# Performance work log

Hardware: AMD Instinct MI355X
Metric: run time of the kernel (lower is better)

The kernel has to match this reference:

```python
import jax, jax.numpy as jnp
import numpy as np

N_NODES = 50000
N_EDGES = 800000
F_IN = 128
HID = 32
HEADS = 4
N_CLASSES = 16
N_GRAPHS = 64
EPS = 1e-5
NEG_SLOPE = 0.2


def setup_inputs() -> dict:
    key = jax.random.key(0)
    ks = jax.random.split(key, 12)
    x = jax.random.normal(ks[0], (N_NODES, F_IN), dtype=jnp.float32)
    edge_index = jax.random.randint(ks[1], (2, N_EDGES), 0, N_NODES, dtype=jnp.int64)
    batch = jnp.sort(jax.random.randint(ks[2], (N_NODES,), 0, N_GRAPHS, dtype=jnp.int64))
    # GATConv 1: F_IN -> HID per head, HEADS heads, concat
    W1 = jax.random.normal(ks[3], (F_IN, HEADS * HID), dtype=jnp.float32) / np.sqrt(F_IN)
    att_src1 = jax.random.normal(ks[4], (HEADS, HID), dtype=jnp.float32) / np.sqrt(HID)
    att_dst1 = jax.random.normal(ks[5], (HEADS, HID), dtype=jnp.float32) / np.sqrt(HID)
    bias1 = jnp.zeros((HEADS * HID,), dtype=jnp.float32)
    # GATConv 2: HEADS*HID -> N_CLASSES, 1 head, no concat
    W2 = jax.random.normal(ks[6], (HEADS * HID, N_CLASSES), dtype=jnp.float32) / np.sqrt(HEADS * HID)
    att_src2 = jax.random.normal(ks[7], (1, N_CLASSES), dtype=jnp.float32) / np.sqrt(N_CLASSES)
    att_dst2 = jax.random.normal(ks[8], (1, N_CLASSES), dtype=jnp.float32) / np.sqrt(N_CLASSES)
    bias2 = jnp.zeros((N_CLASSES,), dtype=jnp.float32)
    # BatchNorm affine params
    bn1_gamma = jnp.ones((F_IN,), dtype=jnp.float32)
    bn1_beta = jnp.zeros((F_IN,), dtype=jnp.float32)
    bn2_gamma = jnp.ones((HEADS * HID,), dtype=jnp.float32)
    bn2_beta = jnp.zeros((HEADS * HID,), dtype=jnp.float32)
    return dict(x=x, W1=W1, att_src1=att_src1, att_dst1=att_dst1, bias1=bias1,
                W2=W2, att_src2=att_src2, att_dst2=att_dst2, bias2=bias2,
                bn1_gamma=bn1_gamma, bn1_beta=bn1_beta,
                bn2_gamma=bn2_gamma, bn2_beta=bn2_beta,
                edge_index=edge_index, batch=batch)


def batchnorm(x, gamma, beta):
    mean = x.mean(axis=0)
    var = ((x - mean) ** 2).mean(axis=0)  # biased var, as torch BN uses for normalization
    return (x - mean) * jax.lax.rsqrt(var + EPS) * gamma + beta


def gat_conv(x, ei, W, a_src, a_dst, bias, heads, out_c, concat):
    N = x.shape[0]
    # add self loops (PyG default)
    loops = jnp.arange(N, dtype=ei.dtype)
    src = jnp.concatenate([ei[0], loops])
    dst = jnp.concatenate([ei[1], loops])
    h = (x @ W).reshape(N, heads, out_c)               # [N,H,C]
    a_s = (h * a_src).sum(-1)                          # [N,H]
    a_d = (h * a_dst).sum(-1)                          # [N,H]
    e = jax.nn.leaky_relu(a_s[src] + a_d[dst], NEG_SLOPE)  # [E,H]
    # softmax over incoming edges of each destination node
    emax = jax.ops.segment_max(e, dst, num_segments=N)[dst]
    ex = jnp.exp(e - emax)
    denom = jax.ops.segment_sum(ex, dst, num_segments=N)[dst]
    alpha = ex / denom                                  # [E,H]
    msg = h[src] * alpha[:, :, None]                    # [E,H,C]
    out = jax.ops.segment_sum(msg, dst, num_segments=N)  # [N,H,C]
    out = out.reshape(N, heads * out_c) if concat else out.mean(axis=1)
    return out + bias


def reference(x, W1, att_src1, att_dst1, bias1, W2, att_src2, att_dst2, bias2,
              bn1_gamma, bn1_beta, bn2_gamma, bn2_beta, edge_index, batch):
    h = batchnorm(x, bn1_gamma, bn1_beta)
    h = gat_conv(h, edge_index, W1, att_src1, att_dst1, bias1, HEADS, HID, True)
    h = jax.nn.relu(h)
    h = batchnorm(h, bn2_gamma, bn2_beta)
    h = gat_conv(h, edge_index, W2, att_src2, att_dst2, bias2, 1, N_CLASSES, False)
    h = jax.nn.gelu(h)
    # global mean pool over graphs
    sums = jax.ops.segment_sum(h, batch, num_segments=N_GRAPHS)
    counts = jax.ops.segment_sum(jnp.ones((h.shape[0],), h.dtype), batch, num_segments=N_GRAPHS)
    pooled = sums / jnp.maximum(counts, 1.0)[:, None]
    return jax.nn.log_softmax(pooled, axis=1)
```

## Files before the change

kernel.cpp:

```cpp
#include <hip/hip_runtime.h>
#include <math.h>
#include <stdint.h>

#define NN 50000
#define NE 800000
#define NG 64
#define NEG_SLOPE 0.2f
#define NBLK ((NN + 255) / 256)

typedef unsigned short u16;
typedef __attribute__((ext_vector_type(8))) unsigned short ushort8;
typedef __attribute__((ext_vector_type(8))) short short8v;
typedef __attribute__((ext_vector_type(4))) float f32x4;

__device__ __forceinline__ float lrelu(float x) { return x > 0.f ? x : NEG_SLOPE * x; }
__device__ __forceinline__ float bf2f(u16 u) { return __uint_as_float(((unsigned)u) << 16); }
__device__ __forceinline__ u16 f2bf(float f) {
    unsigned b = __float_as_uint(f);
    return (u16)((b + 0x7FFF + ((b >> 16) & 1)) >> 16);
}

__global__ __launch_bounds__(256) void col_stats_kernel(const float* __restrict__ X, int nrows,
                                                        float* __restrict__ sum, float* __restrict__ ssum) {
    int tid = threadIdx.x;
    int c = tid & 127, half = tid >> 7;
    int rows_per = (nrows + gridDim.x - 1) / gridDim.x;
    int r0 = blockIdx.x * rows_per;
    int r1 = r0 + rows_per; if (r1 > nrows) r1 = nrows;
    float s = 0.f, ss = 0.f;
    for (int r = r0 + half; r < r1; r += 2) {
        float v = X[(size_t)r * 128 + c];
        s += v; ss += v * v;
    }
    __shared__ float sm1[256], sm2[256];
    sm1[tid] = s; sm2[tid] = ss;
    __syncthreads();
    if (tid < 128) {
        s = sm1[tid] + sm1[tid + 128];
        ss = sm2[tid] + sm2[tid + 128];
        atomicAdd(&sum[c], s);
        atomicAdd(&ssum[c], ss);
    }
}

__global__ __launch_bounds__(128) void bn_prep1_kernel(const float* __restrict__ sum, const float* __restrict__ ssum,
                                                       const float* __restrict__ gamma, const float* __restrict__ beta,
                                                       const float* __restrict__ W, float inv_n,
                                                       u16* __restrict__ WpT, float* __restrict__ hb) {
    int k = threadIdx.x;
    float mean = sum[k] * inv_n;
    float var = ssum[k] * inv_n - mean * mean;
    float a = gamma[k] * rsqrtf(var + 1e-5f);
    float b = beta[k] - mean * a;
    for (int j = 0; j < 128; j++) WpT[j * 128 + k] = f2bf(a * W[k * 128 + j]);
    __shared__ float bs[128];
    bs[k] = b;
    __syncthreads();
    float acc = 0.f;
    for (int kk = 0; kk < 128; kk++) acc += bs[kk] * W[kk * 128 + k];
    hb[k] = acc;
}

__global__ __launch_bounds__(128) void bn_prep_kernel(const float* __restrict__ sum, const float* __restrict__ ssum,
                                                      const float* __restrict__ gamma, const float* __restrict__ beta,
                                                      const float* __restrict__ W, int J, float inv_n,
                                                      float* __restrict__ Wp, float* __restrict__ hb) {
    int k = threadIdx.x;
    float mean = sum[k] * inv_n;
    float var = ssum[k] * inv_n - mean * mean;
    float a = gamma[k] * rsqrtf(var + 1e-5f);
    float b = beta[k] - mean * a;
    for (int j = 0; j < J; j++) Wp[k * J + j] = a * W[k * J + j];
    __shared__ float bs[128];
    bs[k] = b;
    __syncthreads();
    if (k < J) {
        float acc = 0.f;
        for (int kk = 0; kk < 128; kk++) acc += bs[kk] * W[kk * J + k];
        hb[k] = acc;
    }
}

__global__ __launch_bounds__(256) void gemm1_mfma_kernel(const float* __restrict__ X, const u16* __restrict__ WpT,
                                                         const float* __restrict__ hbias, const float* __restrict__ atts,
                                                         const float* __restrict__ attd, u16* __restrict__ Hb,
                                                         float* __restrict__ as_o, float* __restrict__ ad_o) {
    __shared__ u16 wlds[128][136];
    int tid = threadIdx.x;
    for (int u = tid; u < 2048; u += 256) {
        int c = u >> 4, ch = u & 15;
        *(ushort8*)&wlds[c][ch * 8] = *(const ushort8*)&WpT[c * 128 + ch * 8];
    }
    int lane = tid & 63;
    int wv = tid >> 6;
    int cl = lane & 15;
    int kg = lane >> 4;
    int row_base = blockIdx.x * 64 + wv * 16;
    int rr = min(row_base + cl, NN - 1);

    short8v afrag[4];
#pragma unroll
    for (int kb = 0; kb < 4; kb++) {
        const float* xp = &X[(size_t)rr * 128 + kb * 32 + kg * 8];
        float4 x0 = *(const float4*)xp;
        float4 x1 = *(const float4*)(xp + 4);
        ushort8 t;
        t[0] = f2bf(x0.x); t[1] = f2bf(x0.y); t[2] = f2bf(x0.z); t[3] = f2bf(x0.w);
        t[4] = f2bf(x1.x); t[5] = f2bf(x1.y); t[6] = f2bf(x1.z); t[7] = f2bf(x1.w);
        afrag[kb] = (short8v)t;
    }
    __syncthreads();

    f32x4 acc[8];
#pragma unroll
    for (int ct = 0; ct < 8; ct++) {
        f32x4 a = {0.f, 0.f, 0.f, 0.f};
#pragma unroll
        for (int kb = 0; kb < 4; kb++) {
            ushort8 bv = *(const ushort8*)&wlds[ct * 16 + cl][kb * 32 + kg * 8];
            a = __builtin_amdgcn_mfma_f32_16x16x32_bf16(afrag[kb], (short8v)bv, a, 0, 0, 0);
        }
        acc[ct] = a;
    }

#pragma unroll
    for (int reg = 0; reg < 4; reg++) {
        int r = row_base + kg * 4 + reg;
        bool valid = (r < NN);
        float sp[4] = {0.f, 0.f, 0.f, 0.f}, dp[4] = {0.f, 0.f, 0.f, 0.f};
#pragma unroll
        for (int ct = 0; ct < 8; ct++) {
            int c = ct * 16 + cl;
            float v = acc[ct][reg] + hbias[c];
            if (valid) Hb[(size_t)r * 128 + c] = f2bf(v);
            sp[ct >> 1] += v * atts[c];
            dp[ct >> 1] += v * attd[c];
        }
#pragma unroll
        for (int off = 1; off < 16; off <<= 1) {
#pragma unroll
            for (int h = 0; h < 4; h++) {
                sp[h] += __shfl_xor(sp[h], off);
                dp[h] += __shfl_xor(dp[h], off);
            }
        }
        if (valid) {
            if (cl < 4) as_o[r * 4 + cl] = sp[cl];
            else if (cl < 8) ad_o[r * 4 + (cl - 4)] = dp[cl - 4];
        }
    }
}

__global__ __launch_bounds__(256) void deg_hist_kernel(const int* __restrict__ dst, int* __restrict__ deg, int ne) {
    int e = blockIdx.x * 256 + threadIdx.x;
    if (e < ne) atomicAdd(&deg[dst[e]], 1);
}

__global__ __launch_bounds__(256) void scan_part_kernel(const int* __restrict__ deg, int* __restrict__ blocksum) {
    int i = blockIdx.x * 256 + threadIdx.x;
    int d = (i < NN) ? deg[i] : 0;
#pragma unroll
    for (int off = 1; off < 64; off <<= 1) d += __shfl_xor(d, off);
    __shared__ int sm[4];
    if ((threadIdx.x & 63) == 0) sm[threadIdx.x >> 6] = d;
    __syncthreads();
    if (threadIdx.x == 0) blocksum[blockIdx.x] = sm[0] + sm[1] + sm[2] + sm[3];
}

__global__ __launch_bounds__(256) void scan_block_kernel(const int* __restrict__ blocksum, int* __restrict__ blockoff) {
    __shared__ int sm[256];
    int tid = threadIdx.x;
    int v = (tid < NBLK) ? blocksum[tid] : 0;
    sm[tid] = v;
    __syncthreads();
    for (int off = 1; off < 256; off <<= 1) {
        int t = (tid >= off) ? sm[tid - off] : 0;
        __syncthreads();
        sm[tid] += t;
        __syncthreads();
    }
    if (tid < NBLK) blockoff[tid] = sm[tid] - v;
}

__global__ __launch_bounds__(256) void scan_final_kernel(const int* __restrict__ deg, const int* __restrict__ blockoff,
                                                         int* __restrict__ rowptr, int* __restrict__ cursor) {
    __shared__ int sm[256];
    int tid = threadIdx.x;
    int i = blockIdx.x * 256 + tid;
    int d = (i < NN) ? deg[i] : 0;
    sm[tid] = d;
    __syncthreads();
    for (int off = 1; off < 256; off <<= 1) {
        int t = (tid >= off) ? sm[tid - off] : 0;
        __syncthreads();
        sm[tid] += t;
        __syncthreads();
    }
    int excl = sm[tid] - d + blockoff[blockIdx.x];
    if (i < NN) { rowptr[i] = excl; cursor[i] = excl; }
    if (i == NN - 1) rowptr[NN] = excl + d;
}

__global__ __launch_bounds__(256) void scatter_kernel(const int* __restrict__ src, const int* __restrict__ dst,
                                                      int* __restrict__ cursor, int* __restrict__ csr_src, int ne) {
    int e = blockIdx.x * 256 + threadIdx.x;
    if (e < ne) {
        int d = dst[e];
        int pos = atomicAdd(&cursor[d], 1);
        csr_src[pos] = src[e];
    }
}

__global__ __launch_bounds__(256) void gat1_agg_kernel(const u16* __restrict__ Hb, const float* __restrict__ as1,
                                                       const float* __restrict__ ad1, const int* __restrict__ rowptr,
                                                       const int* __restrict__ csr_src, const float* __restrict__ bias1,
                                                       float* __restrict__ out) {
    int n = blockIdx.x * 4 + (threadIdx.x >> 6);
    int lane = threadIdx.x & 63;
    int quarter = lane >> 4;
    int within = lane & 15;
    int head = within >> 2;
    int c8 = within * 8;
    int start = rowptr[n], end = rowptr[n + 1];

    float4 ad4 = *(const float4*)&ad1[n * 4];
    float4 as4 = *(const float4*)&as1[n * 4];
    float ps0 = __expf(lrelu(as4.x + ad4.x));
    float ps1 = __expf(lrelu(as4.y + ad4.y));
    float ps2 = __expf(lrelu(as4.z + ad4.z));
    float ps3 = __expf(lrelu(as4.w + ad4.w));
    float pselfh = (head == 0) ? ps0 : (head == 1) ? ps1 : (head == 2) ? ps2 : ps3;

    float acc[8];
    {
        ushort8 hv = *(const ushort8*)&Hb[(size_t)n * 128 + c8];
        float w = (quarter == 0) ? pselfh : 0.f;
#pragma unroll
        for (int k = 0; k < 8; k++) acc[k] = w * bf2f(hv[k]);
    }
    float d0 = 0.f, d1 = 0.f, d2 = 0.f, d3 = 0.f;

    for (int base = start; base < end; base += 64) {
        int i = base + lane;
        int s = 0;
        float p0 = 0.f, p1 = 0.f, p2 = 0.f, p3 = 0.f;
        if (i < end) {
            s = csr_src[i];
            float4 a = *(const float4*)&as1[(size_t)s * 4];
            p0 = __expf(lrelu(a.x + ad4.x));
            p1 = __expf(lrelu(a.y + ad4.y));
            p2 = __expf(lrelu(a.z + ad4.z));
            p3 = __expf(lrelu(a.w + ad4.w));
            d0 += p0; d1 += p1; d2 += p2; d3 += p3;
        }
        int cnt = min(64, end - base);
#pragma unroll 2
        for (int j = 0; j < cnt; j += 4) {
            int jj = j + quarter;
            int s0 = __shfl(s, jj);
            float q0 = __shfl(p0, jj);
            float q1 = __shfl(p1, jj);
            float q2 = __shfl(p2, jj);
            float q3 = __shfl(p3, jj);
            float pp = (head == 0) ? q0 : (head == 1) ? q1 : (head == 2) ? q2 : q3;
            if (jj < cnt) {
                ushort8 hv = *(const ushort8*)&Hb[(size_t)s0 * 128 + c8];
#pragma unroll
                for (int k = 0; k < 8; k++) acc[k] += pp * bf2f(hv[k]);
            }
        }
    }

#pragma unroll
    for (int off = 1; off < 64; off <<= 1) {
        d0 += __shfl_xor(d0, off);
        d1 += __shfl_xor(d1, off);
        d2 += __shfl_xor(d2, off);
        d3 += __shfl_xor(d3, off);
    }
    float den = ((head == 0) ? d0 : (head == 1) ? d1 : (head == 2) ? d2 : d3) + pselfh;
#pragma unroll
    for (int k = 0; k < 8; k++) {
        acc[k] += __shfl_xor(acc[k], 16);
        acc[k] += __shfl_xor(acc[k], 32);
    }
    if (quarter == 0) {
        float inv = 1.f / den;
        float4 b0 = *(const float4*)&bias1[c8];
        float4 b1 = *(const float4*)&bias1[c8 + 4];
        float4 o0, o1;
        o0.x = fmaxf(acc[0] * inv + b0.x, 0.f);
        o0.y = fmaxf(acc[1] * inv + b0.y, 0.f);
        o0.z = fmaxf(acc[2] * inv + b0.z, 0.f);
        o0.w = fmaxf(acc[3] * inv + b0.w, 0.f);
        o1.x = fmaxf(acc[4] * inv + b1.x, 0.f);
        o1.y = fmaxf(acc[5] * inv + b1.y, 0.f);
        o1.z = fmaxf(acc[6] * inv + b1.z, 0.f);
        o1.w = fmaxf(acc[7] * inv + b1.w, 0.f);
        *(float4*)&out[(size_t)n * 128 + c8] = o0;
        *(float4*)&out[(size_t)n * 128 + c8 + 4] = o1;
    }
}

__global__ __launch_bounds__(256) void gemm2_kernel(const float* __restrict__ X, const float* __restrict__ Wp,
                                                    const float* __restrict__ hb, const float* __restrict__ atts,
                                                    const float* __restrict__ attd, float* __restrict__ H2,
                                                    float* __restrict__ as_o, float* __restrict__ ad_o) {
    __shared__ float xs[16][129];
    __shared__ float wsm[128][16];
    __shared__ float hbs[16], ats[16], atd[16];
    int tid = threadIdx.x;
    if (tid < 16) { hbs[tid] = hb[tid]; ats[tid] = atts[tid]; atd[tid] = attd[tid]; }
    for (int u = tid; u < 2048; u += 256) wsm[u >> 4][u & 15] = Wp[u];
    int r0 = blockIdx.x * 16;
    for (int u = tid; u < 2048; u += 256) {
        int row = u >> 7, cc = u & 127;
        xs[row][cc] = X[(size_t)(r0 + row) * 128 + cc];
    }
    __syncthreads();
    int r = tid >> 4, c = tid & 15;
    float acc = 0.f;
#pragma unroll 8
    for (int k = 0; k < 128; k++) acc += xs[r][k] * wsm[k][c];
    acc += hbs[c];
    H2[(size_t)(r0 + r) * 16 + c] = acc;
    float s = acc * ats[c], d = acc * atd[c];
#pragma unroll
    for (int off = 1; off < 16; off <<= 1) {
        s += __shfl_xor(s, off);
        d += __shfl_xor(d, off);
    }
    if (c == 0) { as_o[r0 + r] = s; ad_o[r0 + r] = d; }
}

__global__ __launch_bounds__(256) void gat2_agg_kernel(const float* __restrict__ H2, const float* __restrict__ as2,
                                                       const float* __restrict__ ad2, const int* __restrict__ rowptr,
                                                       const int* __restrict__ csr_src, const float* __restrict__ bias2,
                                                       float* __restrict__ out) {
    int n = blockIdx.x * 4 + (threadIdx.x >> 6);
    int lane = threadIdx.x & 63;
    int quarter = lane >> 4;
    int c = lane & 15;
    int start = rowptr[n], end = rowptr[n + 1];
    float adn = ad2[n], asn = as2[n];
    float pself = __expf(lrelu(asn + adn));

    float acc = (quarter == 0) ? pself * H2[(size_t)n * 16 + c] : 0.f;
    float d = 0.f;

    for (int base = start; base < end; base += 64) {
        int i = base + lane;
        int s = 0;
        float p = 0.f;
        if (i < end) {
            s = csr_src[i];
            p = __expf(lrelu(as2[s] + adn));
            d += p;
        }
        int cnt = min(64, end - base);
#pragma unroll 2
        for (int j = 0; j < cnt; j += 4) {
            int jj = j + quarter;
            int s0 = __shfl(s, jj);
            float q = __shfl(p, jj);
            if (jj < cnt) acc += q * H2[(size_t)s0 * 16 + c];
        }
    }
#pragma unroll
    for (int off = 1; off < 64; off <<= 1) d += __shfl_xor(d, off);
    float den = d + pself;
    acc += __shfl_xor(acc, 16);
    acc += __shfl_xor(acc, 32);

    if (quarter == 0) {
        float xo = acc / den + bias2[c];
        float t = tanhf(0.7978845608028654f * (xo + 0.044715f * xo * xo * xo));
        out[(size_t)n * 16 + c] = 0.5f * xo * (1.f + t);
    }
}

__global__ __launch_bounds__(256) void pool_lsm_kernel(const float* __restrict__ X, const int* __restrict__ batch,
                                                       int nn, float* __restrict__ out) {
    int g = blockIdx.x;
    int tid = threadIdx.x;
    int lo = 0, hi = nn;
    while (lo < hi) { int mid = (lo + hi) >> 1; if (batch[mid] < g) lo = mid + 1; else hi = mid; }
    int s = lo;
    lo = s; hi = nn;
    while (lo < hi) { int mid = (lo + hi) >> 1; if (batch[mid] < g + 1) lo = mid + 1; else hi = mid; }
    int e2 = lo;
    int c = tid & 15, grp = tid >> 4;
    float acc = 0.f;
    for (int r = s + grp; r < e2; r += 16) acc += X[(size_t)r * 16 + c];
    __shared__ float sm[256];
    sm[tid] = acc;
    __syncthreads();
    for (int off = 8; off >= 1; off >>= 1) {
        if (grp < off) sm[tid] += sm[tid + off * 16];
        __syncthreads();
    }
    if (tid < 16) {
        float cnt = (float)(e2 - s);
        float v = sm[tid] / fmaxf(cnt, 1.f);
        float mx = v;
        mx = fmaxf(mx, __shfl_xor(mx, 1));
        mx = fmaxf(mx, __shfl_xor(mx, 2));
        mx = fmaxf(mx, __shfl_xor(mx, 4));
        mx = fmaxf(mx, __shfl_xor(mx, 8));
        float ex = __expf(v - mx);
        float ssum = ex;
        ssum += __shfl_xor(ssum, 1);
        ssum += __shfl_xor(ssum, 2);
        ssum += __shfl_xor(ssum, 4);
        ssum += __shfl_xor(ssum, 8);
        out[g * 16 + tid] = v - mx - __logf(ssum);
    }
}

extern "C" void kernel_launch(void* const* d_in, const int* in_sizes, int n_in,
                              void* d_out, int out_size, void* d_ws, size_t ws_size,
                              hipStream_t stream) {
    const float* x        = (const float*)d_in[0];
    const float* W1       = (const float*)d_in[1];
    const float* att_src1 = (const float*)d_in[2];
    const float* att_dst1 = (const float*)d_in[3];
    const float* bias1    = (const float*)d_in[4];
    const float* W2       = (const float*)d_in[5];
    const float* att_src2 = (const float*)d_in[6];
    const float* att_dst2 = (const float*)d_in[7];
    const float* bias2    = (const float*)d_in[8];
    const float* bn1g     = (const float*)d_in[9];
    const float* bn1b     = (const float*)d_in[10];
    const float* bn2g     = (const float*)d_in[11];
    const float* bn2b     = (const float*)d_in[12];
    const int*   ei       = (const int*)d_in[13];
    const int*   batch    = (const int*)d_in[14];
    float* out = (float*)d_out;

    char* p = (char*)d_ws;
    auto alloc = [&](size_t bytes) -> char* {
        char* r = p;
        p += (bytes + 255) & ~(size_t)255;
        return r;
    };
    float* bnbuf   = (float*)alloc(512 * sizeof(float));
    int*   deg     = (int*)alloc(NN * sizeof(int));
    int*   rowptr  = (int*)alloc((NN + 1) * sizeof(int));
    int*   cursor  = (int*)alloc(NN * sizeof(int));
    int*   csr_src = (int*)alloc(NE * sizeof(int));
    int*   blocksum= (int*)alloc(NBLK * sizeof(int));
    int*   blockoff= (int*)alloc(NBLK * sizeof(int));
    u16*   W1pT    = (u16*)alloc(128 * 128 * sizeof(u16));
    float* h1bias  = (float*)alloc(128 * sizeof(float));
    u16*   h1b     = (u16*)alloc((size_t)NN * 128 * sizeof(u16));
    float* as1     = (float*)alloc((size_t)NN * 4 * sizeof(float));
    float* ad1     = (float*)alloc((size_t)NN * 4 * sizeof(float));
    float* out1    = (float*)alloc((size_t)NN * 128 * sizeof(float));
    float* W2p     = (float*)alloc(128 * 16 * sizeof(float));
    float* h2bias  = (float*)alloc(16 * sizeof(float));
    float* h2      = (float*)alloc((size_t)NN * 16 * sizeof(float));
    float* as2     = (float*)alloc(NN * sizeof(float));
    float* ad2     = (float*)alloc(NN * sizeof(float));
    float* out2g   = (float*)alloc((size_t)NN * 16 * sizeof(float));

    float* bn1sum = bnbuf;
    float* bn1ss  = bnbuf + 128;
    float* bn2sum = bnbuf + 256;
    float* bn2ss  = bnbuf + 384;
    const int* esrc = ei;
    const int* edst = ei + NE;

    hipMemsetAsync(bnbuf, 0, 512 * sizeof(float) + NN * sizeof(int), stream);

    const float inv_n = 1.f / (float)NN;

    col_stats_kernel<<<256, 256, 0, stream>>>(x, NN, bn1sum, bn1ss);
    bn_prep1_kernel<<<1, 128, 0, stream>>>(bn1sum, bn1ss, bn1g, bn1b, W1, inv_n, W1pT, h1bias);
    gemm1_mfma_kernel<<<(NN + 63) / 64, 256, 0, stream>>>(x, W1pT, h1bias, att_src1, att_dst1, h1b, as1, ad1);
    deg_hist_kernel<<<(NE + 255) / 256, 256, 0, stream>>>(edst, deg, NE);
    scan_part_kernel<<<NBLK, 256, 0, stream>>>(deg, blocksum);
    scan_block_kernel<<<1, 256, 0, stream>>>(blocksum, blockoff);
    scan_final_kernel<<<NBLK, 256, 0, stream>>>(deg, blockoff, rowptr, cursor);
    scatter_kernel<<<(NE + 255) / 256, 256, 0, stream>>>(esrc, edst, cursor, csr_src, NE);
    gat1_agg_kernel<<<NN / 4, 256, 0, stream>>>(h1b, as1, ad1, rowptr, csr_src, bias1, out1);
    col_stats_kernel<<<256, 256, 0, stream>>>(out1, NN, bn2sum, bn2ss);
    bn_prep_kernel<<<1, 128, 0, stream>>>(bn2sum, bn2ss, bn2g, bn2b, W2, 16, inv_n, W2p, h2bias);
    gemm2_kernel<<<NN / 16, 256, 0, stream>>>(out1, W2p, h2bias, att_src2, att_dst2, h2, as2, ad2);
    gat2_agg_kernel<<<NN / 4, 256, 0, stream>>>(h2, as2, ad2, rowptr, csr_src, bias2, out2g);
    pool_lsm_kernel<<<NG, 256, 0, stream>>>(out2g, batch, NN, out);
}
```

Before: 376.9 us.

## Build CSR with two-pass bucketed partition instead of global atomic scatter

Result: faster. 351.9 us (-6.6%).

```diff
diff --git a/kernel.cpp b/kernel.cpp
--- a/kernel.cpp
+++ b/kernel.cpp
@@ -7,6 +7,8 @@
 #define NG 64
 #define NEG_SLOPE 0.2f
 #define NBLK ((NN + 255) / 256)
+#define BSH 8
+#define NBUCK ((NN + 255) >> 8)
 
 typedef unsigned short u16;
 typedef __attribute__((ext_vector_type(8))) unsigned short ushort8;
@@ -183,7 +185,7 @@
 }
 
 __global__ __launch_bounds__(256) void scan_final_kernel(const int* __restrict__ deg, const int* __restrict__ blockoff,
-                                                         int* __restrict__ rowptr, int* __restrict__ cursor) {
+                                                         int* __restrict__ rowptr, int* __restrict__ bcur) {
     __shared__ int sm[256];
     int tid = threadIdx.x;
     int i = blockIdx.x * 256 + tid;
@@ -197,17 +199,52 @@
         __syncthreads();
     }
     int excl = sm[tid] - d + blockoff[blockIdx.x];
-    if (i < NN) { rowptr[i] = excl; cursor[i] = excl; }
+    if (i < NN) {
+        rowptr[i] = excl;
+        if ((i & 255) == 0) bcur[i >> BSH] = excl;
+    }
     if (i == NN - 1) rowptr[NN] = excl + d;
 }
 
-__global__ __launch_bounds__(256) void scatter_kernel(const int* __restrict__ src, const int* __restrict__ dst,
-                                                      int* __restrict__ cursor, int* __restrict__ csr_src, int ne) {
-    int e = blockIdx.x * 256 + threadIdx.x;
-    if (e < ne) {
-        int d = dst[e];
-        int pos = atomicAdd(&cursor[d], 1);
-        csr_src[pos] = src[e];
+__global__ __launch_bounds__(256) void partition_kernel(const int* __restrict__ esrc, const int* __restrict__ edst,
+                                                        int* __restrict__ bcur, int2* __restrict__ ebuf) {
+    __shared__ int hist[NBUCK];
+    __shared__ int cur[NBUCK];
+    int tid = threadIdx.x;
+    for (int b = tid; b < NBUCK; b += 256) hist[b] = 0;
+    __syncthreads();
+    int epb = (NE + gridDim.x - 1) / gridDim.x;
+    int e0 = blockIdx.x * epb;
+    int e1 = min(e0 + epb, NE);
+    for (int e = e0 + tid; e < e1; e += 256)
+        atomicAdd(&hist[edst[e] >> BSH], 1);
+    __syncthreads();
+    for (int b = tid; b < NBUCK; b += 256) {
+        int h = hist[b];
+        cur[b] = h ? atomicAdd(&bcur[b], h) : 0;
+    }
+    __syncthreads();
+    for (int e = e0 + tid; e < e1; e += 256) {
+        int s = esrc[e], d = edst[e];
+        int pos = atomicAdd(&cur[d >> BSH], 1);
+        ebuf[pos] = make_int2(s, d);
+    }
+}
+
+__global__ __launch_bounds__(256) void fine_scatter_kernel(const int2* __restrict__ ebuf, const int* __restrict__ rowptr,
+                                                           int* __restrict__ csr_src) {
+    __shared__ int lcur[256];
+    int b = blockIdx.x;
+    int n0 = b << BSH;
+    int n1 = min(n0 + 256, NN);
+    int tid = threadIdx.x;
+    if (n0 + tid < n1) lcur[tid] = rowptr[n0 + tid];
+    __syncthreads();
+    int e0 = rowptr[n0], e1 = rowptr[n1];
+    for (int e = e0 + tid; e < e1; e += 256) {
+        int2 p = ebuf[e];
+        int pos = atomicAdd(&lcur[p.y - n0], 1);
+        csr_src[pos] = p.x;
     }
 }
 
@@ -446,8 +483,9 @@
     float* bnbuf   = (float*)alloc(512 * sizeof(float));
     int*   deg     = (int*)alloc(NN * sizeof(int));
     int*   rowptr  = (int*)alloc((NN + 1) * sizeof(int));
-    int*   cursor  = (int*)alloc(NN * sizeof(int));
+    int*   bcur    = (int*)alloc(NBUCK * sizeof(int));
     int*   csr_src = (int*)alloc(NE * sizeof(int));
+    int2*  ebuf    = (int2*)alloc((size_t)NE * sizeof(int2));
     int*   blocksum= (int*)alloc(NBLK * sizeof(int));
     int*   blockoff= (int*)alloc(NBLK * sizeof(int));
     u16*   W1pT    = (u16*)alloc(128 * 128 * sizeof(u16));
@@ -480,8 +518,9 @@
     deg_hist_kernel<<<(NE + 255) / 256, 256, 0, stream>>>(edst, deg, NE);
     scan_part_kernel<<<NBLK, 256, 0, stream>>>(deg, blocksum);
     scan_block_kernel<<<1, 256, 0, stream>>>(blocksum, blockoff);
-    scan_final_kernel<<<NBLK, 256, 0, stream>>>(deg, blockoff, rowptr, cursor);
-    scatter_kernel<<<(NE + 255) / 256, 256, 0, stream>>>(esrc, edst, cursor, csr_src, NE);
+    scan_final_kernel<<<NBLK, 256, 0, stream>>>(deg, blockoff, rowptr, bcur);
+    partition_kernel<<<256, 256, 0, stream>>>(esrc, edst, bcur, ebuf);
+    fine_scatter_kernel<<<NBUCK, 256, 0, stream>>>(ebuf, rowptr, csr_src);
     gat1_agg_kernel<<<NN / 4, 256, 0, stream>>>(h1b, as1, ad1, rowptr, csr_src, bias1, out1);
     col_stats_kernel<<<256, 256, 0, stream>>>(out1, NN, bn2sum, bn2ss);
     bn_prep_kernel<<<1, 128, 0, stream>>>(bn2sum, bn2ss, bn2g, bn2b, W2, 16, inv_n, W2p, h2bias);
```
